# Kernel tuning notes

Hardware: AMD Instinct MI355X
Metric: run time of the kernel (lower is better)

The kernel has to match this reference:

```python
import jax, jax.numpy as jnp
import numpy as np

N, E, IN_DIM, HID, H, D = 50000, 800000, 1280, 256, 4, 64  # gat_out_dim = H*D = HID
NEG_SLOPE = 0.2


def setup_inputs() -> dict:
    key = jax.random.key(0)
    ks = jax.random.split(key, 20)

    def lin(k, fi, fo):
        return (jax.random.normal(k, (fi, fo), jnp.float32) / np.float32(np.sqrt(fi)))

    inp = {
        "x": jax.random.normal(ks[0], (N, IN_DIM), jnp.float32),
        "edge_index": jax.random.randint(ks[1], (2, E), 0, N, dtype=jnp.int32),
        "enc_W": lin(ks[2], IN_DIM, HID), "enc_b": jnp.zeros((HID,), jnp.float32),
        "Wl0": lin(ks[3], HID, H * D), "bl0": jnp.zeros((H * D,), jnp.float32),
        "Wr0": lin(ks[4], HID, H * D), "br0": jnp.zeros((H * D,), jnp.float32),
        "att0": jax.random.normal(ks[5], (H, D), jnp.float32) / np.float32(np.sqrt(D)),
        "bias0": jnp.zeros((H * D,), jnp.float32),
        "Wl1": lin(ks[6], HID, H * D), "bl1": jnp.zeros((H * D,), jnp.float32),
        "Wr1": lin(ks[7], HID, H * D), "br1": jnp.zeros((H * D,), jnp.float32),
        "att1": jax.random.normal(ks[8], (H, D), jnp.float32) / np.float32(np.sqrt(D)),
        "bias1": jnp.zeros((H * D,), jnp.float32),
        "clf_W": lin(ks[9], HID, 1), "clf_b": jnp.zeros((1,), jnp.float32),
    }
    return inp


def gatv2_layer(x, src, dst, Wl, bl, Wr, br, att, bias):
    # x: [N, HID]; src/dst: [E'] with self-loops already appended
    xl = (x @ Wl + bl).reshape(N, H, D)  # source transform
    xr = (x @ Wr + br).reshape(N, H, D)  # target transform
    e = jax.nn.leaky_relu(xl[src] + xr[dst], NEG_SLOPE)   # [E', H, D]
    logits = jnp.einsum('ehd,hd->eh', e, att)              # [E', H]
    # segment softmax over destination nodes (every node has a self-loop)
    m = jax.ops.segment_max(logits, dst, num_segments=N)   # [N, H]
    a = jnp.exp(logits - m[dst])
    denom = jax.ops.segment_sum(a, dst, num_segments=N)
    alpha = a / (denom[dst] + 1e-16)                       # [E', H]
    out = jax.ops.segment_sum(xl[src] * alpha[:, :, None], dst, num_segments=N)
    out = out.reshape(N, H * D) + bias
    out = out + x  # residual (in_dim == out_features -> identity residual); dropout is eval-mode no-op
    return jax.nn.elu(out), alpha


def reference(x, edge_index, enc_W, enc_b, Wl0, bl0, Wr0, br0, att0, bias0,
              Wl1, bl1, Wr1, br1, att1, bias1, clf_W, clf_b):
    # add self loops (PyG GATv2Conv default)
    loops = jnp.arange(N, dtype=edge_index.dtype)
    src = jnp.concatenate([edge_index[0], loops])
    dst = jnp.concatenate([edge_index[1], loops])

    h = x @ enc_W + enc_b                                  # node encoder [N, HID]
    h, alpha0 = gatv2_layer(h, src, dst, Wl0, bl0, Wr0, br0, att0, bias0)
    h, alpha1 = gatv2_layer(h, src, dst, Wl1, bl1, Wr1, br1, att1, bias1)
    preds = (h @ clf_W + clf_b).squeeze(-1)                # [N]
    return preds, alpha0, alpha1
```

## Files before the change

kernel.cpp:

```cpp
#include <hip/hip_runtime.h>
#include <hip/hip_bf16.h>
#include <math.h>

#define N_NODES 50000
#define E_EDGES 800000
#define EP (E_EDGES + N_NODES)
#define IN_DIM 1280
#define HID 256
#define NHEAD 4
#define DHEAD 64
#define NEG_SLOPE 0.2f

typedef unsigned short ushort_t;
typedef __attribute__((ext_vector_type(8))) short short8;
typedef __attribute__((ext_vector_type(4))) float floatx4;

__device__ __forceinline__ float bf2f(ushort_t h) {
  return __uint_as_float(((unsigned)h) << 16);
}
__device__ __forceinline__ void split_bf16(float x, ushort_t& hi, ushort_t& lo) {
  unsigned u = __float_as_uint(x);
  hi = (ushort_t)(u >> 16);
  float rem = x - __uint_as_float(u & 0xFFFF0000u);
  lo = (ushort_t)(__float_as_uint(rem) >> 16);
}

__device__ __forceinline__ void gload_lds16(const void* g, void* l) {
  __builtin_amdgcn_global_load_lds(
      (const __attribute__((address_space(1))) unsigned int*)g,
      (__attribute__((address_space(3))) unsigned int*)l, 16, 0, 0);
}


__global__ void hist_kernel(const int* __restrict__ ei, int* __restrict__ deg) {
  int e = blockIdx.x * blockDim.x + threadIdx.x;
  if (e >= EP) return;
  int dst = (e < E_EDGES) ? ei[E_EDGES + e] : (e - E_EDGES);
  atomicAdd(&deg[dst], 1);
}

__global__ __launch_bounds__(1024) void scan_kernel(int* __restrict__ dc, int* __restrict__ row_ptr) {
  __shared__ int wsum[16];
  int tid = threadIdx.x;
  int lane = tid & 63;
  int wid = tid >> 6;
  int running = 0;
  if (tid == 0) row_ptr[0] = 0;
  for (int base = 0; base < N_NODES; base += 1024) {
    int i = base + tid;
    int v = (i < N_NODES) ? dc[i] : 0;
    int s = v;
    #pragma unroll
    for (int off = 1; off < 64; off <<= 1) {
      int t = __shfl_up(s, off);
      if (lane >= off) s += t;
    }
    if (lane == 63) wsum[wid] = s;
    __syncthreads();
    if (wid == 0 && lane < 16) {
      int w = wsum[lane];
      #pragma unroll
      for (int off = 1; off < 16; off <<= 1) {
        int t = __shfl_up(w, off);
        if (lane >= off) w += t;
      }
      wsum[lane] = w;
    }
    __syncthreads();
    int woff = (wid > 0) ? wsum[wid - 1] : 0;
    int incl = running + woff + s;
    if (i < N_NODES) {
      row_ptr[i + 1] = incl;
      dc[i] = incl - v;
    }
    running += wsum[15];
    __syncthreads();
  }
}

__global__ void scatter_kernel(const int* __restrict__ ei, int* __restrict__ cursor,
                               int* __restrict__ csr_src, int* __restrict__ csr_eid) {
  int e = blockIdx.x * blockDim.x + threadIdx.x;
  if (e >= EP) return;
  int src, dst;
  if (e < E_EDGES) { src = ei[e]; dst = ei[E_EDGES + e]; }
  else             { src = dst = e - E_EDGES; }
  int pos = atomicAdd(&cursor[dst], 1);
  csr_src[pos] = src;
  csr_eid[pos] = e;
}

__global__ void wsplit_kernel(const float* __restrict__ W, ushort_t* __restrict__ WhT,
                              ushort_t* __restrict__ WlT, int K, int Nc) {
  int idx = blockIdx.x * blockDim.x + threadIdx.x;
  if (idx >= K * Nc) return;
  int k = idx / Nc, n = idx - k * Nc;
  ushort_t hi, lo;
  split_bf16(W[idx], hi, lo);
  WhT[(size_t)n * K + k] = hi;
  WlT[(size_t)n * K + k] = lo;
}

__global__ __launch_bounds__(256) void gemm_mfma(const float* __restrict__ A,
                                                 const ushort_t* __restrict__ BhT,
                                                 const ushort_t* __restrict__ BlT,
                                                 const float* __restrict__ bias,
                                                 float* __restrict__ C,
                                                 int M, int K, int Nc) {
  __shared__ ushort_t sAh[128 * 32];
  __shared__ ushort_t sAl[128 * 32];
  __shared__ ushort_t sBh[128 * 32];
  __shared__ ushort_t sBl[128 * 32];

  const int tid = threadIdx.x;
  const int lane = tid & 63;
  const int w = tid >> 6;
  const int wm = w >> 1, wn = w & 1;
  const int bm = blockIdx.x * 128;
  const int bn = blockIdx.y * 128;
  const int r = lane & 15, q = lane >> 4;

  const int ar = tid >> 1;
  const int ahalf = tid & 1;
  int arow = bm + ar; if (arow >= M) arow = M - 1;
  const float* aptr = A + (size_t)arow * K + ahalf * 16;

  floatx4 acc[4][4];
  #pragma unroll
  for (int i = 0; i < 4; ++i)
    #pragma unroll
    for (int j = 0; j < 4; ++j) acc[i][j] = (floatx4)(0.0f);

  const int e0 = tid, e1 = tid + 256;
  const size_t b0off = (size_t)(bn + (e0 >> 2)) * K + (e0 & 3) * 8;
  const size_t b1off = (size_t)(bn + (e1 >> 2)) * K + (e1 & 3) * 8;

  for (int k0 = 0; k0 < K; k0 += 32) {
    gload_lds16(BhT + b0off + k0, &sBh[e0 * 8]);
    gload_lds16(BhT + b1off + k0, &sBh[e1 * 8]);
    gload_lds16(BlT + b0off + k0, &sBl[e0 * 8]);
    gload_lds16(BlT + b1off + k0, &sBl[e1 * 8]);

    float va[16];
    *(float4*)&va[0]  = *(const float4*)(aptr + k0);
    *(float4*)&va[4]  = *(const float4*)(aptr + k0 + 4);
    *(float4*)&va[8]  = *(const float4*)(aptr + k0 + 8);
    *(float4*)&va[12] = *(const float4*)(aptr + k0 + 12);
    short8 h0, h1, l0, l1;
    #pragma unroll
    for (int i = 0; i < 8; ++i) {
      ushort_t hi, lo;
      split_bf16(va[i], hi, lo);
      h0[i] = (short)hi; l0[i] = (short)lo;
    }
    #pragma unroll
    for (int i = 0; i < 8; ++i) {
      ushort_t hi, lo;
      split_bf16(va[8 + i], hi, lo);
      h1[i] = (short)hi; l1[i] = (short)lo;
    }
    int aoff = ar * 32 + ahalf * 16;
    *(short8*)&sAh[aoff] = h0;  *(short8*)&sAh[aoff + 8] = h1;
    *(short8*)&sAl[aoff] = l0;  *(short8*)&sAl[aoff + 8] = l1;

    __syncthreads();

    short8 ah[4], al[4], bh[4], bl[4];
    #pragma unroll
    for (int i = 0; i < 4; ++i) {
      int arow_l = (wm * 64 + i * 16 + r) * 32 + q * 8;
      int brow_l = (wn * 64 + i * 16 + r) * 32 + q * 8;
      ah[i] = *(const short8*)&sAh[arow_l];
      al[i] = *(const short8*)&sAl[arow_l];
      bh[i] = *(const short8*)&sBh[brow_l];
      bl[i] = *(const short8*)&sBl[brow_l];
    }
    #pragma unroll
    for (int i = 0; i < 4; ++i)
      #pragma unroll
      for (int j = 0; j < 4; ++j) {
        acc[i][j] = __builtin_amdgcn_mfma_f32_16x16x32_bf16(ah[i], bh[j], acc[i][j], 0, 0, 0);
        acc[i][j] = __builtin_amdgcn_mfma_f32_16x16x32_bf16(ah[i], bl[j], acc[i][j], 0, 0, 0);
        acc[i][j] = __builtin_amdgcn_mfma_f32_16x16x32_bf16(al[i], bh[j], acc[i][j], 0, 0, 0);
      }
    __syncthreads();
  }

  #pragma unroll
  for (int j = 0; j < 4; ++j) {
    int col = bn + wn * 64 + j * 16 + r;
    float bv = bias[col];
    #pragma unroll
    for (int i = 0; i < 4; ++i) {
      int row0 = bm + wm * 64 + i * 16 + q * 4;
      #pragma unroll
      for (int rr = 0; rr < 4; ++rr) {
        int row = row0 + rr;
        if (row < M) C[(size_t)row * Nc + col] = acc[i][j][rr] + bv;
      }
    }
  }
}

__global__ __launch_bounds__(64) void gat_layer(const float* __restrict__ xl,
                                                const float* __restrict__ xr,
                                                float* h_inout,
                                                const float* __restrict__ att,
                                                const float* __restrict__ bias,
                                                const int* __restrict__ row_ptr,
                                                const int* __restrict__ csr_src,
                                                const int* __restrict__ csr_eid,
                                                float* __restrict__ logits_ws,
                                                float* __restrict__ alpha_out) {
  int node = blockIdx.x;
  int l = threadIdx.x;
  int hgrp = l >> 4;
  int r0 = row_ptr[node];
  int r1 = row_ptr[node + 1];

  float4 xr4 = *(const float4*)(xr + (size_t)node * HID + l * 4);
  float4 at4 = *(const float4*)(att + l * 4);

  float m = -INFINITY;
  float den = 0.f;
  float4 acc = make_float4(0.f, 0.f, 0.f, 0.f);
  for (int j = r0; j < r1; ++j) {
    int s = csr_src[j];
    float4 v = *(const float4*)(xl + (size_t)s * HID + l * 4);
    float t0 = v.x + xr4.x; t0 = (t0 > 0.f) ? t0 : NEG_SLOPE * t0;
    float t1 = v.y + xr4.y; t1 = (t1 > 0.f) ? t1 : NEG_SLOPE * t1;
    float t2 = v.z + xr4.z; t2 = (t2 > 0.f) ? t2 : NEG_SLOPE * t2;
    float t3 = v.w + xr4.w; t3 = (t3 > 0.f) ? t3 : NEG_SLOPE * t3;
    float p = t0 * at4.x + t1 * at4.y + t2 * at4.z + t3 * at4.w;
    p += __shfl_xor(p, 1);
    p += __shfl_xor(p, 2);
    p += __shfl_xor(p, 4);
    p += __shfl_xor(p, 8);
    if ((l & 15) == 0) logits_ws[(size_t)j * NHEAD + hgrp] = p;
    float m_new = fmaxf(m, p);
    float scale = __expf(m - m_new);
    float wgt = __expf(p - m_new);
    den = den * scale + wgt;
    acc.x = acc.x * scale + wgt * v.x;
    acc.y = acc.y * scale + wgt * v.y;
    acc.z = acc.z * scale + wgt * v.z;
    acc.w = acc.w * scale + wgt * v.w;
    m = m_new;
  }
  float inv_den = 1.f / (den + 1e-16f);

  float4 b4 = *(const float4*)(bias + l * 4);
  float4 h4 = *(const float4*)(h_inout + (size_t)node * HID + l * 4);
  float o0 = acc.x * inv_den + b4.x + h4.x;
  float o1 = acc.y * inv_den + b4.y + h4.y;
  float o2 = acc.z * inv_den + b4.z + h4.z;
  float o3 = acc.w * inv_den + b4.w + h4.w;
  o0 = (o0 > 0.f) ? o0 : (__expf(o0) - 1.f);
  o1 = (o1 > 0.f) ? o1 : (__expf(o1) - 1.f);
  o2 = (o2 > 0.f) ? o2 : (__expf(o2) - 1.f);
  o3 = (o3 > 0.f) ? o3 : (__expf(o3) - 1.f);
  *(float4*)(h_inout + (size_t)node * HID + l * 4) = make_float4(o0, o1, o2, o3);

  __threadfence_block();

  float mh = __shfl(m, (l & 3) * 16);
  float dh = __shfl(den, (l & 3) * 16);
  float invd = 1.f / (dh + 1e-16f);
  for (int j = r0 + (l >> 2); j < r1; j += 16) {
    float lg = logits_ws[(size_t)j * NHEAD + (l & 3)];
    alpha_out[(size_t)csr_eid[j] * NHEAD + (l & 3)] = __expf(lg - mh) * invd;
  }
}

__global__ __launch_bounds__(64) void clf_kernel(const float* __restrict__ h,
                                                 const float* __restrict__ clf_W,
                                                 const float* __restrict__ clf_b,
                                                 float* __restrict__ preds) {
  int n = blockIdx.x;
  int l = threadIdx.x;
  float4 v = *(const float4*)(h + (size_t)n * HID + l * 4);
  float4 w = *(const float4*)(clf_W + l * 4);
  float s = v.x * w.x + v.y * w.y + v.z * w.z + v.w * w.w;
  s += __shfl_xor(s, 1);
  s += __shfl_xor(s, 2);
  s += __shfl_xor(s, 4);
  s += __shfl_xor(s, 8);
  s += __shfl_xor(s, 16);
  s += __shfl_xor(s, 32);
  if (l == 0) preds[n] = s + clf_b[0];
}

static inline char* carve(char*& p, size_t bytes) {
  char* ret = p;
  p += (bytes + 255) & ~(size_t)255;
  return ret;
}

extern "C" void kernel_launch(void* const* d_in, const int* in_sizes, int n_in,
                              void* d_out, int out_size, void* d_ws, size_t ws_size,
                              hipStream_t stream) {
  const float* x     = (const float*)d_in[0];
  const int*   ei    = (const int*)d_in[1];
  const float* enc_W = (const float*)d_in[2];
  const float* enc_b = (const float*)d_in[3];
  const float* Wl0   = (const float*)d_in[4];
  const float* bl0   = (const float*)d_in[5];
  const float* Wr0   = (const float*)d_in[6];
  const float* br0   = (const float*)d_in[7];
  const float* att0  = (const float*)d_in[8];
  const float* bias0 = (const float*)d_in[9];
  const float* Wl1   = (const float*)d_in[10];
  const float* bl1   = (const float*)d_in[11];
  const float* Wr1   = (const float*)d_in[12];
  const float* br1   = (const float*)d_in[13];
  const float* att1  = (const float*)d_in[14];
  const float* bias1 = (const float*)d_in[15];
  const float* clf_W = (const float*)d_in[16];
  const float* clf_b = (const float*)d_in[17];

  float* preds  = (float*)d_out;
  float* alpha0 = preds + N_NODES;
  float* alpha1 = alpha0 + (size_t)EP * NHEAD;

  char* p = (char*)d_ws;
  float* h      = (float*)carve(p, (size_t)N_NODES * HID * 4);
  float* xl     = (float*)carve(p, (size_t)N_NODES * HID * 4);
  float* xr     = (float*)carve(p, (size_t)N_NODES * HID * 4);
  float* logits = (float*)carve(p, (size_t)EP * NHEAD * 4);
  int* row_ptr  = (int*)carve(p, (size_t)(N_NODES + 1) * 4);
  int* cursor   = (int*)carve(p, (size_t)N_NODES * 4);
  int* csr_src  = (int*)carve(p, (size_t)EP * 4);
  int* csr_eid  = (int*)carve(p, (size_t)EP * 4);
  ushort_t* encWh = (ushort_t*)carve(p, (size_t)IN_DIM * HID * 2);
  ushort_t* encWl = (ushort_t*)carve(p, (size_t)IN_DIM * HID * 2);
  ushort_t* Wl0h  = (ushort_t*)carve(p, (size_t)HID * HID * 2);
  ushort_t* Wl0l  = (ushort_t*)carve(p, (size_t)HID * HID * 2);
  ushort_t* Wr0h  = (ushort_t*)carve(p, (size_t)HID * HID * 2);
  ushort_t* Wr0l  = (ushort_t*)carve(p, (size_t)HID * HID * 2);
  ushort_t* Wl1h  = (ushort_t*)carve(p, (size_t)HID * HID * 2);
  ushort_t* Wl1l  = (ushort_t*)carve(p, (size_t)HID * HID * 2);
  ushort_t* Wr1h  = (ushort_t*)carve(p, (size_t)HID * HID * 2);
  ushort_t* Wr1l  = (ushort_t*)carve(p, (size_t)HID * HID * 2);

  hipMemsetAsync(cursor, 0, N_NODES * sizeof(int), stream);
  int eb = 256, eg = (EP + eb - 1) / eb;
  hist_kernel<<<eg, eb, 0, stream>>>(ei, cursor);
  scan_kernel<<<1, 1024, 0, stream>>>(cursor, row_ptr);
  scatter_kernel<<<eg, eb, 0, stream>>>(ei, cursor, csr_src, csr_eid);

  int wthreads = 256;
  wsplit_kernel<<<(IN_DIM * HID + wthreads - 1) / wthreads, wthreads, 0, stream>>>(enc_W, encWh, encWl, IN_DIM, HID);
  wsplit_kernel<<<(HID * HID + wthreads - 1) / wthreads, wthreads, 0, stream>>>(Wl0, Wl0h, Wl0l, HID, HID);
  wsplit_kernel<<<(HID * HID + wthreads - 1) / wthreads, wthreads, 0, stream>>>(Wr0, Wr0h, Wr0l, HID, HID);
  wsplit_kernel<<<(HID * HID + wthreads - 1) / wthreads, wthreads, 0, stream>>>(Wl1, Wl1h, Wl1l, HID, HID);
  wsplit_kernel<<<(HID * HID + wthreads - 1) / wthreads, wthreads, 0, stream>>>(Wr1, Wr1h, Wr1l, HID, HID);

  dim3 gGemm((N_NODES + 127) / 128, HID / 128);
  dim3 bGemm(256);

  gemm_mfma<<<gGemm, bGemm, 0, stream>>>(x, encWh, encWl, enc_b, h, N_NODES, IN_DIM, HID);

  gemm_mfma<<<gGemm, bGemm, 0, stream>>>(h, Wl0h, Wl0l, bl0, xl, N_NODES, HID, HID);
  gemm_mfma<<<gGemm, bGemm, 0, stream>>>(h, Wr0h, Wr0l, br0, xr, N_NODES, HID, HID);
  gat_layer<<<N_NODES, 64, 0, stream>>>(xl, xr, h, att0, bias0, row_ptr, csr_src, csr_eid, logits, alpha0);

  gemm_mfma<<<gGemm, bGemm, 0, stream>>>(h, Wl1h, Wl1l, bl1, xl, N_NODES, HID, HID);
  gemm_mfma<<<gGemm, bGemm, 0, stream>>>(h, Wr1h, Wr1l, br1, xr, N_NODES, HID, HID);
  gat_layer<<<N_NODES, 64, 0, stream>>>(xl, xr, h, att1, bias1, row_ptr, csr_src, csr_eid, logits, alpha1);

  clf_kernel<<<N_NODES, 64, 0, stream>>>(h, clf_W, clf_b, preds);
}
```

Measured before the change: 1.145 ms.

## Fuse Wl/Wr GEMMs, use 64-row tiles and k-packed B layout

Concatenates the Wl and Wr weight matrices into one packed B operand so each GAT layer runs a single GEMM with twice the columns, reading h once instead of twice. The GEMM tile shrinks from 128 to 64 rows, with padded A rows in LDS to avoid bank conflicts and an occupancy hint of 4 blocks per CU. B is stored k-chunk-major, which makes the LDS fragment reads contiguous. The smaller tile doubles the number of blocks, which helps fill the machine, but halves register reuse per block.

```diff
diff --git a/kernel.cpp b/kernel.cpp
--- a/kernel.cpp
+++ b/kernel.cpp
@@ -15,9 +15,6 @@
 typedef __attribute__((ext_vector_type(8))) short short8;
 typedef __attribute__((ext_vector_type(4))) float floatx4;
 
-__device__ __forceinline__ float bf2f(ushort_t h) {
-  return __uint_as_float(((unsigned)h) << 16);
-}
 __device__ __forceinline__ void split_bf16(float x, ushort_t& hi, ushort_t& lo) {
   unsigned u = __float_as_uint(x);
   hi = (ushort_t)(u >> 16);
@@ -90,25 +87,28 @@
   csr_eid[pos] = e;
 }
 
-__global__ void wsplit_kernel(const float* __restrict__ W, ushort_t* __restrict__ WhT,
-                              ushort_t* __restrict__ WlT, int K, int Nc) {
+__global__ void wsplit_packed(const float* __restrict__ W, ushort_t* __restrict__ Ph,
+                              ushort_t* __restrict__ Pl, int K, int Nc, int NcT, int colOff) {
   int idx = blockIdx.x * blockDim.x + threadIdx.x;
   if (idx >= K * Nc) return;
   int k = idx / Nc, n = idx - k * Nc;
   ushort_t hi, lo;
   split_bf16(W[idx], hi, lo);
-  WhT[(size_t)n * K + k] = hi;
-  WlT[(size_t)n * K + k] = lo;
-}
-
-__global__ __launch_bounds__(256) void gemm_mfma(const float* __restrict__ A,
-                                                 const ushort_t* __restrict__ BhT,
-                                                 const ushort_t* __restrict__ BlT,
-                                                 const float* __restrict__ bias,
-                                                 float* __restrict__ C,
-                                                 int M, int K, int Nc) {
-  __shared__ ushort_t sAh[128 * 32];
-  __shared__ ushort_t sAl[128 * 32];
+  size_t pi = ((size_t)(k >> 3) * NcT + colOff + n) * 8 + (k & 7);
+  Ph[pi] = hi;
+  Pl[pi] = lo;
+}
+
+__global__ __launch_bounds__(256, 4) void gemm64(const float* __restrict__ A,
+                                                 const ushort_t* __restrict__ Bh,
+                                                 const ushort_t* __restrict__ Bl,
+                                                 const float* __restrict__ bias_l,
+                                                 const float* __restrict__ bias_r,
+                                                 float* __restrict__ C_l,
+                                                 float* __restrict__ C_r,
+                                                 int M, int K, int NcT, int Nsplit) {
+  __shared__ ushort_t sAh[64 * 40];
+  __shared__ ushort_t sAl[64 * 40];
   __shared__ ushort_t sBh[128 * 32];
   __shared__ ushort_t sBl[128 * 32];
 
@@ -116,67 +116,62 @@
   const int lane = tid & 63;
   const int w = tid >> 6;
   const int wm = w >> 1, wn = w & 1;
-  const int bm = blockIdx.x * 128;
+  const int bm = blockIdx.x * 64;
   const int bn = blockIdx.y * 128;
   const int r = lane & 15, q = lane >> 4;
 
-  const int ar = tid >> 1;
-  const int ahalf = tid & 1;
-  int arow = bm + ar; if (arow >= M) arow = M - 1;
-  const float* aptr = A + (size_t)arow * K + ahalf * 16;
-
-  floatx4 acc[4][4];
+  floatx4 acc[2][4];
   #pragma unroll
-  for (int i = 0; i < 4; ++i)
+  for (int i = 0; i < 2; ++i)
     #pragma unroll
     for (int j = 0; j < 4; ++j) acc[i][j] = (floatx4)(0.0f);
 
+  const int arow = tid >> 2, achunk = tid & 3;
+  int ag = bm + arow; if (ag >= M) ag = M - 1;
+  const float* aptr = A + (size_t)ag * K + achunk * 8;
+  const int awoff = arow * 40 + achunk * 8;
+
   const int e0 = tid, e1 = tid + 256;
-  const size_t b0off = (size_t)(bn + (e0 >> 2)) * K + (e0 & 3) * 8;
-  const size_t b1off = (size_t)(bn + (e1 >> 2)) * K + (e1 & 3) * 8;
+  const size_t b0base = ((size_t)(e0 >> 7) * NcT + bn + (e0 & 127)) * 8;
+  const size_t b1base = ((size_t)(e1 >> 7) * NcT + bn + (e1 & 127)) * 8;
 
   for (int k0 = 0; k0 < K; k0 += 32) {
-    gload_lds16(BhT + b0off + k0, &sBh[e0 * 8]);
-    gload_lds16(BhT + b1off + k0, &sBh[e1 * 8]);
-    gload_lds16(BlT + b0off + k0, &sBl[e0 * 8]);
-    gload_lds16(BlT + b1off + k0, &sBl[e1 * 8]);
-
-    float va[16];
-    *(float4*)&va[0]  = *(const float4*)(aptr + k0);
-    *(float4*)&va[4]  = *(const float4*)(aptr + k0 + 4);
-    *(float4*)&va[8]  = *(const float4*)(aptr + k0 + 8);
-    *(float4*)&va[12] = *(const float4*)(aptr + k0 + 12);
-    short8 h0, h1, l0, l1;
+    size_t kadd = (size_t)(k0 >> 3) * NcT * 8;
+    gload_lds16(Bh + b0base + kadd, &sBh[e0 * 8]);
+    gload_lds16(Bh + b1base + kadd, &sBh[e1 * 8]);
+    gload_lds16(Bl + b0base + kadd, &sBl[e0 * 8]);
+    gload_lds16(Bl + b1base + kadd, &sBl[e1 * 8]);
+
+    float va[8];
+    *(float4*)&va[0] = *(const float4*)(aptr + k0);
+    *(float4*)&va[4] = *(const float4*)(aptr + k0 + 4);
+    short8 hv, lv;
     #pragma unroll
     for (int i = 0; i < 8; ++i) {
       ushort_t hi, lo;
       split_bf16(va[i], hi, lo);
-      h0[i] = (short)hi; l0[i] = (short)lo;
-    }
-    #pragma unroll
-    for (int i = 0; i < 8; ++i) {
-      ushort_t hi, lo;
-      split_bf16(va[8 + i], hi, lo);
-      h1[i] = (short)hi; l1[i] = (short)lo;
-    }
-    int aoff = ar * 32 + ahalf * 16;
-    *(short8*)&sAh[aoff] = h0;  *(short8*)&sAh[aoff + 8] = h1;
-    *(short8*)&sAl[aoff] = l0;  *(short8*)&sAl[aoff + 8] = l1;
-
-    __syncthreads();
-
-    short8 ah[4], al[4], bh[4], bl[4];
-    #pragma unroll
-    for (int i = 0; i < 4; ++i) {
-      int arow_l = (wm * 64 + i * 16 + r) * 32 + q * 8;
-      int brow_l = (wn * 64 + i * 16 + r) * 32 + q * 8;
-      ah[i] = *(const short8*)&sAh[arow_l];
-      al[i] = *(const short8*)&sAl[arow_l];
-      bh[i] = *(const short8*)&sBh[brow_l];
-      bl[i] = *(const short8*)&sBl[brow_l];
-    }
-    #pragma unroll
-    for (int i = 0; i < 4; ++i)
+      hv[i] = (short)hi; lv[i] = (short)lo;
+    }
+    *(short8*)&sAh[awoff] = hv;
+    *(short8*)&sAl[awoff] = lv;
+
+    __syncthreads();
+
+    short8 ah[2], al[2], bh[4], bl[4];
+    #pragma unroll
+    for (int i = 0; i < 2; ++i) {
+      int off = (wm * 32 + i * 16 + r) * 40 + q * 8;
+      ah[i] = *(const short8*)&sAh[off];
+      al[i] = *(const short8*)&sAl[off];
+    }
+    #pragma unroll
+    for (int j = 0; j < 4; ++j) {
+      int off = (q * 128 + wn * 64 + j * 16 + r) * 8;
+      bh[j] = *(const short8*)&sBh[off];
+      bl[j] = *(const short8*)&sBl[off];
+    }
+    #pragma unroll
+    for (int i = 0; i < 2; ++i)
       #pragma unroll
       for (int j = 0; j < 4; ++j) {
         acc[i][j] = __builtin_amdgcn_mfma_f32_16x16x32_bf16(ah[i], bh[j], acc[i][j], 0, 0, 0);
@@ -188,15 +183,18 @@
 
   #pragma unroll
   for (int j = 0; j < 4; ++j) {
-    int col = bn + wn * 64 + j * 16 + r;
-    float bv = bias[col];
-    #pragma unroll
-    for (int i = 0; i < 4; ++i) {
-      int row0 = bm + wm * 64 + i * 16 + q * 4;
+    int cg = bn + wn * 64 + j * 16 + r;
+    bool sec = cg >= Nsplit;
+    int cc = sec ? cg - Nsplit : cg;
+    float bv = sec ? bias_r[cc] : bias_l[cc];
+    float* Cb = sec ? C_r : C_l;
+    #pragma unroll
+    for (int i = 0; i < 2; ++i) {
+      int row0 = bm + wm * 32 + i * 16 + q * 4;
       #pragma unroll
       for (int rr = 0; rr < 4; ++rr) {
         int row = row0 + rr;
-        if (row < M) C[(size_t)row * Nc + col] = acc[i][j][rr] + bv;
+        if (row < M) Cb[(size_t)row * HID + cc] = acc[i][j][rr] + bv;
       }
     }
   }
@@ -331,16 +329,12 @@
   int* cursor   = (int*)carve(p, (size_t)N_NODES * 4);
   int* csr_src  = (int*)carve(p, (size_t)EP * 4);
   int* csr_eid  = (int*)carve(p, (size_t)EP * 4);
-  ushort_t* encWh = (ushort_t*)carve(p, (size_t)IN_DIM * HID * 2);
-  ushort_t* encWl = (ushort_t*)carve(p, (size_t)IN_DIM * HID * 2);
-  ushort_t* Wl0h  = (ushort_t*)carve(p, (size_t)HID * HID * 2);
-  ushort_t* Wl0l  = (ushort_t*)carve(p, (size_t)HID * HID * 2);
-  ushort_t* Wr0h  = (ushort_t*)carve(p, (size_t)HID * HID * 2);
-  ushort_t* Wr0l  = (ushort_t*)carve(p, (size_t)HID * HID * 2);
-  ushort_t* Wl1h  = (ushort_t*)carve(p, (size_t)HID * HID * 2);
-  ushort_t* Wl1l  = (ushort_t*)carve(p, (size_t)HID * HID * 2);
-  ushort_t* Wr1h  = (ushort_t*)carve(p, (size_t)HID * HID * 2);
-  ushort_t* Wr1l  = (ushort_t*)carve(p, (size_t)HID * HID * 2);
+  ushort_t* encPh = (ushort_t*)carve(p, (size_t)IN_DIM * HID * 2);
+  ushort_t* encPl = (ushort_t*)carve(p, (size_t)IN_DIM * HID * 2);
+  ushort_t* P0h   = (ushort_t*)carve(p, (size_t)HID * 512 * 2);
+  ushort_t* P0l   = (ushort_t*)carve(p, (size_t)HID * 512 * 2);
+  ushort_t* P1h   = (ushort_t*)carve(p, (size_t)HID * 512 * 2);
+  ushort_t* P1l   = (ushort_t*)carve(p, (size_t)HID * 512 * 2);
 
   hipMemsetAsync(cursor, 0, N_NODES * sizeof(int), stream);
   int eb = 256, eg = (EP + eb - 1) / eb;
@@ -348,24 +342,25 @@
   scan_kernel<<<1, 1024, 0, stream>>>(cursor, row_ptr);
   scatter_kernel<<<eg, eb, 0, stream>>>(ei, cursor, csr_src, csr_eid);
 
-  int wthreads = 256;
-  wsplit_kernel<<<(IN_DIM * HID + wthreads - 1) / wthreads, wthreads, 0, stream>>>(enc_W, encWh, encWl, IN_DIM, HID);
-  wsplit_kernel<<<(HID * HID + wthreads - 1) / wthreads, wthreads, 0, stream>>>(Wl0, Wl0h, Wl0l, HID, HID);
-  wsplit_kernel<<<(HID * HID + wthreads - 1) / wthreads, wthreads, 0, stream>>>(Wr0, Wr0h, Wr0l, HID, HID);
-  wsplit_kernel<<<(HID * HID + wthreads - 1) / wthreads, wthreads, 0, stream>>>(Wl1, Wl1h, Wl1l, HID, HID);
-  wsplit_kernel<<<(HID * HID + wthreads - 1) / wthreads, wthreads, 0, stream>>>(Wr1, Wr1h, Wr1l, HID, HID);
-
-  dim3 gGemm((N_NODES + 127) / 128, HID / 128);
+  int wt = 256;
+  wsplit_packed<<<(IN_DIM * HID + wt - 1) / wt, wt, 0, stream>>>(enc_W, encPh, encPl, IN_DIM, HID, HID, 0);
+  wsplit_packed<<<(HID * HID + wt - 1) / wt, wt, 0, stream>>>(Wl0, P0h, P0l, HID, HID, 512, 0);
+  wsplit_packed<<<(HID * HID + wt - 1) / wt, wt, 0, stream>>>(Wr0, P0h, P0l, HID, HID, 512, 256);
+  wsplit_packed<<<(HID * HID + wt - 1) / wt, wt, 0, stream>>>(Wl1, P1h, P1l, HID, HID, 512, 0);
+  wsplit_packed<<<(HID * HID + wt - 1) / wt, wt, 0, stream>>>(Wr1, P1h, P1l, HID, HID, 512, 256);
+
+  const int MB = (N_NODES + 63) / 64;
   dim3 bGemm(256);
 
-  gemm_mfma<<<gGemm, bGemm, 0, stream>>>(x, encWh, encWl, enc_b, h, N_NODES, IN_DIM, HID);
-
-  gemm_mfma<<<gGemm, bGemm, 0, stream>>>(h, Wl0h, Wl0l, bl0, xl, N_NODES, HID, HID);
-  gemm_mfma<<<gGemm, bGemm, 0, stream>>>(h, Wr0h, Wr0l, br0, xr, N_NODES, HID, HID);
+  gemm64<<<dim3(MB, 2), bGemm, 0, stream>>>(x, encPh, encPl, enc_b, enc_b, h, h,
+                                            N_NODES, IN_DIM, HID, HID);
+
+  gemm64<<<dim3(MB, 4), bGemm, 0, stream>>>(h, P0h, P0l, bl0, br0, xl, xr,
+                                            N_NODES, HID, 512, HID);
   gat_layer<<<N_NODES, 64, 0, stream>>>(xl, xr, h, att0, bias0, row_ptr, csr_src, csr_eid, logits, alpha0);
 
-  gemm_mfma<<<gGemm, bGemm, 0, stream>>>(h, Wl1h, Wl1l, bl1, xl, N_NODES, HID, HID);
-  gemm_mfma<<<gGemm, bGemm, 0, stream>>>(h, Wr1h, Wr1l, br1, xr, N_NODES, HID, HID);
+  gemm64<<<dim3(MB, 4), bGemm, 0, stream>>>(h, P1h, P1l, bl1, br1, xl, xr,
+                                            N_NODES, HID, 512, HID);
   gat_layer<<<N_NODES, 64, 0, stream>>>(xl, xr, h, att1, bias1, row_ptr, csr_src, csr_eid, logits, alpha1);
 
   clf_kernel<<<N_NODES, 64, 0, stream>>>(h, clf_W, clf_b, preds);
```

New measurement: 1.076 ms. 6.0% less time.
